# Performance work log

Hardware: AMD Instinct MI355X
Metric: run time of the kernel (lower is better)

The kernel has to match this reference:

```python
import jax, jax.numpy as jnp
import numpy as np

N_VIEWS = 3
N = 20000            # samples per omic view
NT = N_VIEWS * N     # homogeneous node count
E = 800000           # number of edges
R = 6                # num_relations
B = 4                # num_bases
H = 1                # heads
D = 128              # proj_dim == hidden_channels
IN_FEAT = 2000
NUM_LABELS = 5
NEG_SLOPE = 0.2      # PyG leaky_relu default slope


def setup_inputs() -> dict:
    key = jax.random.key(0)
    ks = jax.random.split(key, 16)
    inp = {}
    for i in range(N_VIEWS):
        inp[f"x{i}"] = jax.random.normal(ks[i], (N, IN_FEAT), jnp.float32)
        inp[f"w_proj{i}"] = jax.random.normal(ks[3 + i], (IN_FEAT, D), jnp.float32) / np.sqrt(IN_FEAT)
        inp[f"b_proj{i}"] = jnp.zeros((D,), jnp.float32)
    inp["edge_src"] = jax.random.randint(ks[6], (E,), 0, NT, jnp.int32)
    inp["edge_dst"] = jax.random.randint(ks[7], (E,), 0, NT, jnp.int32)
    inp["edge_type"] = jax.random.randint(ks[8], (E,), 0, R, jnp.int32)
    inp["basis"] = jax.random.normal(ks[9], (B, D, H * D), jnp.float32) / np.sqrt(D)
    inp["comp"] = jax.random.normal(ks[10], (R, B), jnp.float32) / np.sqrt(B)
    inp["att_q"] = jax.random.normal(ks[11], (H * D, H), jnp.float32) / np.sqrt(D)
    inp["att_k"] = jax.random.normal(ks[12], (H * D, H), jnp.float32) / np.sqrt(D)
    inp["conv_bias"] = jnp.zeros((H * D,), jnp.float32)
    inp["w_int"] = jax.random.normal(ks[13], (N_VIEWS * H * D, NUM_LABELS), jnp.float32) / np.sqrt(N_VIEWS * D)
    inp["b_int"] = jnp.zeros((NUM_LABELS,), jnp.float32)
    return inp


def rgat_conv(x, edge_src, edge_dst, edge_type, basis, comp, att_q, att_k, bias):
    """PyG RGATConv: basis-decomposed relational transform + additive
    across-relation self-attention (dim=1), sum aggregation, concat heads."""
    e = edge_src.shape[0]
    # relation weights from bases: [R, D, H*D]
    w = jnp.einsum('rb,bio->rio', comp, basis)
    # transform every node under every relation: [R, NT, H*D]
    xw = jnp.einsum('nd,rdo->rno', x, w)
    xi = xw[edge_type, edge_dst]   # [E, H*D] transformed target feats
    xj = xw[edge_type, edge_src]   # [E, H*D] transformed source feats
    q = xi @ att_q                 # [E, H]
    k = xj @ att_k                 # [E, H]
    alpha = jax.nn.leaky_relu(q + k, NEG_SLOPE)
    # softmax over incoming edges of each target node (across relations)
    amax = jax.lax.stop_gradient(jax.ops.segment_max(alpha, edge_dst, num_segments=NT))
    ealpha = jnp.exp(alpha - amax[edge_dst])
    denom = jax.ops.segment_sum(ealpha, edge_dst, num_segments=NT)
    alpha = ealpha / (denom[edge_dst] + 1e-16)
    msg = (xj.reshape(e, H, D) * alpha[:, :, None]).reshape(e, H * D)
    out = jax.ops.segment_sum(msg, edge_dst, num_segments=NT)  # [NT, H*D]
    return out + bias


def reference(x0, x1, x2, w_proj0, b_proj0, w_proj1, b_proj1, w_proj2, b_proj2,
              edge_src, edge_dst, edge_type, basis, comp, att_q, att_k,
              conv_bias, w_int, b_int):
    # per-omic projection + relu, then concat to homogeneous node matrix
    h = jnp.concatenate([
        jax.nn.relu(x0 @ w_proj0 + b_proj0),
        jax.nn.relu(x1 @ w_proj1 + b_proj1),
        jax.nn.relu(x2 @ w_proj2 + b_proj2),
    ], axis=0)                                        # [NT, D]
    h = jax.nn.relu(rgat_conv(h, edge_src, edge_dst, edge_type,
                              basis, comp, att_q, att_k, conv_bias))
    # node-type gather: nodes are ordered by type in the homogeneous graph
    views = h.reshape(N_VIEWS, N, H * D)              # [V, N, D]
    feat = jnp.transpose(views, (1, 0, 2)).reshape(N, N_VIEWS * H * D)
    # LinearIntegration: concat views -> linear to classes
    return feat @ w_int + b_int                        # [N, NUM_LABELS]
```

## Files before the change

kernel.cpp:

```cpp
#include <hip/hip_runtime.h>
#include <hip/hip_bf16.h>

#define NV 3
#define NN 20000
#define NTT 60000
#define NE 800000
#define NR 6
#define NB 4
#define DD 128
#define INF 2000
#define NL 5

typedef __attribute__((ext_vector_type(8))) short short8;
typedef __attribute__((ext_vector_type(4))) float f32x4;

__device__ __forceinline__ unsigned short f2bf(float f) {
    unsigned int u = __float_as_uint(f);
    u += 0x7FFFu + ((u >> 16) & 1u);
    return (unsigned short)(u >> 16);
}
__device__ __forceinline__ float bf2f(unsigned short h) {
    return __uint_as_float(((unsigned int)h) << 16);
}
__device__ __forceinline__ short8 cvt8(float4 a, float4 b) {
    union { short8 v; __hip_bfloat162 h[4]; } u;
    u.h[0] = __float22bfloat162_rn(make_float2(a.x, a.y));
    u.h[1] = __float22bfloat162_rn(make_float2(a.z, a.w));
    u.h[2] = __float22bfloat162_rn(make_float2(b.x, b.y));
    u.h[3] = __float22bfloat162_rn(make_float2(b.z, b.w));
    return u.v;
}

__global__ void prep_misc(const float* __restrict__ basis, const float* __restrict__ comp,
                          const float* __restrict__ att_q, const float* __restrict__ att_k,
                          unsigned short* __restrict__ wTrel, float* __restrict__ qvec,
                          float* __restrict__ kvec, int* __restrict__ indeg,
                          int* __restrict__ cursor) {
    int b = blockIdx.x;
    if (b < 384) {
        int idx = b * 256 + threadIdx.x;
        int r = idx / (DD * DD);
        int rem = idx - r * (DD * DD);
        int o = rem / DD;
        int d = rem - o * DD;
        float s = 0.f;
        #pragma unroll
        for (int bb = 0; bb < NB; bb++)
            s += comp[r * NB + bb] * basis[((size_t)bb * DD + d) * DD + o];
        wTrel[idx] = f2bf(s);
    } else if (b < 390) {
        int idx = (b - 384) * 256 + threadIdx.x;
        int sel = idx / (NR * DD);
        int rem = idx - sel * (NR * DD);
        int r = rem / DD;
        int d = rem - r * DD;
        const float* att = sel ? att_k : att_q;
        float s = 0.f;
        #pragma unroll
        for (int bb = 0; bb < NB; bb++) {
            float cb = comp[r * NB + bb];
            float t = 0.f;
            for (int o = 0; o < DD; o++) t += basis[((size_t)bb * DD + d) * DD + o] * att[o];
            s += cb * t;
        }
        (sel ? kvec : qvec)[r * DD + d] = s;
    } else {
        int i = (b - 390) * 256 + threadIdx.x;
        if (i < NTT) { indeg[i] = 0; cursor[i] = 0; }
    }
}

__global__ void prep_wTt(const float* __restrict__ w0, const float* __restrict__ w1,
                         const float* __restrict__ w2, unsigned short* __restrict__ wT) {
    __shared__ float tile[32][33];
    int v = blockIdx.z;
    const float* w = (v == 0) ? w0 : ((v == 1) ? w1 : w2);
    int k0 = blockIdx.x * 32, n0 = blockIdx.y * 32;
    int tx = threadIdx.x & 31, ty = threadIdx.x >> 5;
    #pragma unroll
    for (int i = 0; i < 4; i++) {
        int k = k0 + ty + i * 8;
        if (k < INF) tile[ty + i * 8][tx] = w[(size_t)k * DD + n0 + tx];
    }
    __syncthreads();
    #pragma unroll
    for (int i = 0; i < 4; i++) {
        int k = k0 + tx;
        int n = n0 + ty + i * 8;
        if (k < INF)
            wT[(size_t)v * DD * INF + (size_t)n * INF + k] = f2bf(tile[tx][ty + i * 8]);
    }
}

__global__ __launch_bounds__(256) void proj_nl(
    const float* __restrict__ x0, const float* __restrict__ x1, const float* __restrict__ x2,
    const float* __restrict__ b0, const float* __restrict__ b1, const float* __restrict__ b2,
    const unsigned short* __restrict__ wT, unsigned short* __restrict__ hout) {
    int v = blockIdx.y;
    const float* x = (v == 0) ? x0 : ((v == 1) ? x1 : x2);
    const float* bias = (v == 0) ? b0 : ((v == 1) ? b1 : b2);
    const unsigned short* wTv = wT + (size_t)v * DD * INF;

    int t = threadIdx.x, lane = t & 63, wid = t >> 6;
    int wm = wid >> 1, wn = wid & 1;
    int lm = lane & 15, lq = lane >> 4;

    const float* aptr[4];
    #pragma unroll
    for (int i = 0; i < 4; i++) {
        int r = blockIdx.x * 128 + wm * 64 + i * 16 + lm;
        if (r >= NN) r = NN - 1;
        aptr[i] = x + (size_t)r * INF + lq * 8;
    }
    const unsigned short* bptr[4];
    #pragma unroll
    for (int j = 0; j < 4; j++) {
        int c = wn * 64 + j * 16 + lm;
        bptr[j] = wTv + (size_t)c * INF + lq * 8;
    }

    f32x4 acc[4][4];
    #pragma unroll
    for (int i = 0; i < 4; i++)
        #pragma unroll
        for (int j = 0; j < 4; j++) {
            acc[i][j][0] = 0.f; acc[i][j][1] = 0.f; acc[i][j][2] = 0.f; acc[i][j][3] = 0.f;
        }

    #pragma unroll 2
    for (int kk = 0; kk < 62; kk++) {
        short8 af[4], bfr[4];
        #pragma unroll
        for (int i = 0; i < 4; i++) {
            const float4* p = (const float4*)(aptr[i] + kk * 32);
            af[i] = cvt8(p[0], p[1]);
        }
        #pragma unroll
        for (int j = 0; j < 4; j++)
            bfr[j] = *(const short8*)(bptr[j] + kk * 32);
        #pragma unroll
        for (int i = 0; i < 4; i++)
            #pragma unroll
            for (int j = 0; j < 4; j++)
                acc[i][j] = __builtin_amdgcn_mfma_f32_16x16x32_bf16(af[i], bfr[j], acc[i][j], 0, 0, 0);
    }
    {
        short8 af[4], bfr[4];
        short8 z = {0, 0, 0, 0, 0, 0, 0, 0};
        #pragma unroll
        for (int i = 0; i < 4; i++) {
            if (lq < 2) {
                const float4* p = (const float4*)(aptr[i] + 62 * 32);
                af[i] = cvt8(p[0], p[1]);
            } else af[i] = z;
        }
        #pragma unroll
        for (int j = 0; j < 4; j++)
            bfr[j] = (lq < 2) ? *(const short8*)(bptr[j] + 62 * 32) : z;
        #pragma unroll
        for (int i = 0; i < 4; i++)
            #pragma unroll
            for (int j = 0; j < 4; j++)
                acc[i][j] = __builtin_amdgcn_mfma_f32_16x16x32_bf16(af[i], bfr[j], acc[i][j], 0, 0, 0);
    }
    #pragma unroll
    for (int i = 0; i < 4; i++) {
        int lr = wm * 64 + i * 16 + lq * 4;
        #pragma unroll
        for (int j = 0; j < 4; j++) {
            int c = wn * 64 + j * 16 + lm;
            float bv = bias[c];
            #pragma unroll
            for (int u = 0; u < 4; u++) {
                int grow = blockIdx.x * 128 + lr + u;
                if (grow < NN) {
                    float o = fmaxf(acc[i][j][u] + bv, 0.f);
                    hout[((size_t)(v * NN + grow)) * DD + c] = f2bf(o);
                }
            }
        }
    }
}

__global__ __launch_bounds__(256) void xw_nl(
    const unsigned short* __restrict__ h, const unsigned short* __restrict__ wTrel,
    unsigned short* __restrict__ xw) {
    int r = blockIdx.y;
    const unsigned short* wTr = wTrel + (size_t)r * DD * DD;
    int t = threadIdx.x, lane = t & 63, wid = t >> 6;
    int wm = wid >> 1, wn = wid & 1;
    int lm = lane & 15, lq = lane >> 4;

    const unsigned short* aptr[4];
    #pragma unroll
    for (int i = 0; i < 4; i++) {
        int rr = blockIdx.x * 128 + wm * 64 + i * 16 + lm;
        if (rr >= NTT) rr = NTT - 1;
        aptr[i] = h + (size_t)rr * DD + lq * 8;
    }
    const unsigned short* bptr[4];
    #pragma unroll
    for (int j = 0; j < 4; j++) {
        int c = wn * 64 + j * 16 + lm;
        bptr[j] = wTr + (size_t)c * DD + lq * 8;
    }

    f32x4 acc[4][4];
    #pragma unroll
    for (int i = 0; i < 4; i++)
        #pragma unroll
        for (int j = 0; j < 4; j++) {
            acc[i][j][0] = 0.f; acc[i][j][1] = 0.f; acc[i][j][2] = 0.f; acc[i][j][3] = 0.f;
        }

    #pragma unroll
    for (int kk = 0; kk < 4; kk++) {
        short8 af[4], bfr[4];
        #pragma unroll
        for (int i = 0; i < 4; i++) af[i] = *(const short8*)(aptr[i] + kk * 32);
        #pragma unroll
        for (int j = 0; j < 4; j++) bfr[j] = *(const short8*)(bptr[j] + kk * 32);
        #pragma unroll
        for (int i = 0; i < 4; i++)
            #pragma unroll
            for (int j = 0; j < 4; j++)
                acc[i][j] = __builtin_amdgcn_mfma_f32_16x16x32_bf16(af[i], bfr[j], acc[i][j], 0, 0, 0);
    }
    #pragma unroll
    for (int i = 0; i < 4; i++) {
        int lr = wm * 64 + i * 16 + lq * 4;
        #pragma unroll
        for (int j = 0; j < 4; j++) {
            int c = wn * 64 + j * 16 + lm;
            #pragma unroll
            for (int u = 0; u < 4; u++) {
                int g2 = blockIdx.x * 128 + lr + u;
                if (g2 < NTT)
                    xw[((size_t)r * NTT + g2) * DD + c] = f2bf(acc[i][j][u]);
            }
        }
    }
}

__global__ void qk_nodes(const unsigned short* __restrict__ h, const float* __restrict__ qvec,
                         const float* __restrict__ kvec, float* __restrict__ qn,
                         float* __restrict__ kn) {
    int wid = threadIdx.x >> 6, lane = threadIdx.x & 63;
    int node = blockIdx.x * 4 + wid;
    if (node >= NTT) return;
    unsigned int u = *(const unsigned int*)(h + (size_t)node * DD + lane * 2);
    float h0 = bf2f(u & 0xffff), h1 = bf2f(u >> 16);
    #pragma unroll
    for (int r = 0; r < NR; r++) {
        float pq = h0 * qvec[r * DD + lane * 2] + h1 * qvec[r * DD + lane * 2 + 1];
        float pk = h0 * kvec[r * DD + lane * 2] + h1 * kvec[r * DD + lane * 2 + 1];
        #pragma unroll
        for (int off = 32; off; off >>= 1) {
            pq += __shfl_xor(pq, off);
            pk += __shfl_xor(pk, off);
        }
        if (lane == 0) {
            qn[r * NTT + node] = pq;
            kn[r * NTT + node] = pk;
        }
    }
}

__global__ void hist(const int* __restrict__ dst, int* __restrict__ indeg) {
    int e = blockIdx.x * 256 + threadIdx.x;
    if (e < NE) atomicAdd(&indeg[dst[e]], 1);
}

__global__ __launch_bounds__(1024) void scan_indeg(const int* __restrict__ indeg,
                                                   int* __restrict__ start) {
    int t = threadIdx.x;
    const int per = (NTT + 1023) / 1024;
    int base = t * per;
    int s = 0;
    for (int i = 0; i < per; i++) {
        int idx = base + i;
        if (idx < NTT) s += indeg[idx];
    }
    int lane = t & 63, wid = t >> 6;
    __shared__ int wsum[16];
    int v = s;
    #pragma unroll
    for (int off = 1; off < 64; off <<= 1) {
        int u = __shfl_up(v, off);
        if (lane >= off) v += u;
    }
    if (lane == 63) wsum[wid] = v;
    __syncthreads();
    if (t < 16) {
        int w = wsum[t];
        #pragma unroll
        for (int off = 1; off < 16; off <<= 1) {
            int u = __shfl_up(w, off);
            if (t >= off) w += u;
        }
        wsum[t] = w;
    }
    __syncthreads();
    int excl = (v - s) + (wid ? wsum[wid - 1] : 0);
    int run = excl;
    for (int i = 0; i < per; i++) {
        int idx = base + i;
        if (idx < NTT) {
            start[idx] = run;
            run += indeg[idx];
        }
    }
    if (t == 1023) start[NTT] = run;
}

__global__ void scatter2(const int* __restrict__ dst, const int* __restrict__ src,
                         const int* __restrict__ typ, const int* __restrict__ start,
                         int* __restrict__ cursor, const float* __restrict__ qn,
                         const float* __restrict__ kn, unsigned int* __restrict__ packed,
                         float* __restrict__ wl) {
    int e = blockIdx.x * 256 + threadIdx.x;
    if (e >= NE) return;
    int d = dst[e], ss = src[e], tt = typ[e];
    float al = qn[tt * NTT + d] + kn[tt * NTT + ss];
    al = (al > 0.f) ? al : 0.2f * al;
    float w = __expf(al);
    int pos = atomicAdd(&cursor[d], 1);
    int idx = start[d] + pos;
    packed[idx] = (unsigned)ss | ((unsigned)tt << 16);
    wl[idx] = w;
}

__global__ void aggregate(const unsigned int* __restrict__ packed, const float* __restrict__ wl,
                          const int* __restrict__ start, const unsigned short* __restrict__ xw,
                          const float* __restrict__ conv_bias, float* __restrict__ h2) {
    int wid = threadIdx.x >> 6, lane = threadIdx.x & 63;
    int node = blockIdx.x * 4 + wid;
    if (node >= NTT) return;
    int s0 = start[node], s1 = start[node + 1];
    float a0 = 0.f, a1 = 0.f, denom = 0.f;
    for (int base = s0; base < s1; base += 64) {
        int cnt = min(64, s1 - base);
        unsigned pk = 0;
        float wv = 0.f;
        if (lane < cnt) {
            pk = packed[base + lane];
            wv = wl[base + lane];
        }
        denom += wv;
        for (int i = 0; i < cnt; i++) {
            unsigned sp = __shfl(pk, i);
            float sw = __shfl(wv, i);
            unsigned ss = sp & 0xFFFFu;
            unsigned tt = sp >> 16;
            unsigned u = *(const unsigned int*)(xw + ((size_t)tt * NTT + ss) * DD + lane * 2);
            a0 += sw * bf2f(u & 0xffff);
            a1 += sw * bf2f(u >> 16);
        }
    }
    #pragma unroll
    for (int off = 32; off; off >>= 1) denom += __shfl_xor(denom, off);
    float rdenom = 1.f / (denom + 1e-16f);
    float2 o;
    o.x = fmaxf(a0 * rdenom + conv_bias[lane * 2], 0.f);
    o.y = fmaxf(a1 * rdenom + conv_bias[lane * 2 + 1], 0.f);
    *(float2*)&h2[(size_t)node * DD + lane * 2] = o;
}

__global__ void final_linear(const float* __restrict__ h2, const float* __restrict__ w_int,
                             const float* __restrict__ b_int, float* __restrict__ out) {
    int wid = threadIdx.x >> 6, lane = threadIdx.x & 63;
    int node = blockIdx.x * 4 + wid;
    if (node >= NN) return;
    float acc[NL] = {0.f, 0.f, 0.f, 0.f, 0.f};
    for (int j = lane; j < NV * DD; j += 64) {
        int v = j >> 7, d = j & 127;
        float f = h2[((size_t)(v * NN + node)) * DD + d];
        #pragma unroll
        for (int c = 0; c < NL; c++) acc[c] += f * w_int[j * NL + c];
    }
    #pragma unroll
    for (int c = 0; c < NL; c++) {
        float s = acc[c];
        #pragma unroll
        for (int off = 32; off; off >>= 1) s += __shfl_xor(s, off);
        if (lane == 0) out[(size_t)node * NL + c] = s + b_int[c];
    }
}

extern "C" void kernel_launch(void* const* d_in, const int* in_sizes, int n_in, void* d_out,
                              int out_size, void* d_ws, size_t ws_size, hipStream_t stream) {
    (void)in_sizes; (void)n_in; (void)out_size; (void)ws_size;
    const float* x0 = (const float*)d_in[0];
    const float* w0 = (const float*)d_in[1];
    const float* b0 = (const float*)d_in[2];
    const float* x1 = (const float*)d_in[3];
    const float* w1 = (const float*)d_in[4];
    const float* b1 = (const float*)d_in[5];
    const float* x2 = (const float*)d_in[6];
    const float* w2 = (const float*)d_in[7];
    const float* b2 = (const float*)d_in[8];
    const int* esrc = (const int*)d_in[9];
    const int* edst = (const int*)d_in[10];
    const int* etype = (const int*)d_in[11];
    const float* basis = (const float*)d_in[12];
    const float* comp = (const float*)d_in[13];
    const float* att_q = (const float*)d_in[14];
    const float* att_k = (const float*)d_in[15];
    const float* conv_bias = (const float*)d_in[16];
    const float* w_int = (const float*)d_in[17];
    const float* b_int = (const float*)d_in[18];

    char* ws = (char*)d_ws;
    size_t off = 0;
    auto alloc = [&](size_t bytes) -> void* {
        void* p = ws + off;
        off += bytes;
        off = (off + 255) & ~(size_t)255;
        return p;
    };
    unsigned short* h = (unsigned short*)alloc((size_t)NTT * DD * 2);
    unsigned short* xw = (unsigned short*)alloc((size_t)NR * NTT * DD * 2);
    float* qn = (float*)alloc((size_t)NR * NTT * 4);
    float* kn = (float*)alloc((size_t)NR * NTT * 4);
    unsigned short* wT = (unsigned short*)alloc((size_t)NV * DD * INF * 2);
    unsigned short* wTrel = (unsigned short*)alloc((size_t)NR * DD * DD * 2);
    float* qvec = (float*)alloc((size_t)NR * DD * 4);
    float* kvec = (float*)alloc((size_t)NR * DD * 4);
    int* indeg = (int*)alloc((size_t)NTT * 4);
    int* cursor = (int*)alloc((size_t)NTT * 4);
    int* startp = (int*)alloc((size_t)(NTT + 1) * 4);
    unsigned int* packed = (unsigned int*)alloc((size_t)NE * 4);
    float* wl = (float*)alloc((size_t)NE * 4);
    float* h2 = (float*)alloc((size_t)NTT * DD * 4);

    prep_misc<<<390 + (NTT + 255) / 256, 256, 0, stream>>>(basis, comp, att_q, att_k, wTrel,
                                                           qvec, kvec, indeg, cursor);
    prep_wTt<<<dim3((INF + 31) / 32, DD / 32, NV), 256, 0, stream>>>(w0, w1, w2, wT);
    hist<<<(NE + 255) / 256, 256, 0, stream>>>(edst, indeg);
    scan_indeg<<<1, 1024, 0, stream>>>(indeg, startp);

    proj_nl<<<dim3((NN + 127) / 128, NV), 256, 0, stream>>>(x0, x1, x2, b0, b1, b2, wT, h);
    qk_nodes<<<(NTT + 3) / 4, 256, 0, stream>>>(h, qvec, kvec, qn, kn);
    xw_nl<<<dim3((NTT + 127) / 128, NR), 256, 0, stream>>>(h, wTrel, xw);

    scatter2<<<(NE + 255) / 256, 256, 0, stream>>>(edst, esrc, etype, startp, cursor, qn, kn,
                                                   packed, wl);
    aggregate<<<(NTT + 3) / 4, 256, 0, stream>>>(packed, wl, startp, xw, conv_bias, h2);
    final_linear<<<(NN + 3) / 4, 256, 0, stream>>>(h2, w_int, b_int, (float*)d_out);
}
```

Before: 948.2 us.

## Halve projection tile rows, prefetch A registers, and coalesce indegree scan

The projection GEMM now uses 64-row blocks instead of 128, doubling the grid (about 939 blocks vs 471) so more CUs stay busy. The fp32 A-operand loads are software-prefetched one k-step ahead in registers to hide global latency behind the MFMAs. The single-block indegree scan is rewritten to process 1024 contiguous elements per round, so loads and stores are coalesced instead of strided per thread. In exchange, each B fragment is reused across fewer rows, which raises weight reads, and the scan adds extra barriers per round.

```diff
diff --git a/kernel.cpp b/kernel.cpp
--- a/kernel.cpp
+++ b/kernel.cpp
@@ -105,10 +105,10 @@
     int wm = wid >> 1, wn = wid & 1;
     int lm = lane & 15, lq = lane >> 4;
 
-    const float* aptr[4];
-    #pragma unroll
-    for (int i = 0; i < 4; i++) {
-        int r = blockIdx.x * 128 + wm * 64 + i * 16 + lm;
+    const float* aptr[2];
+    #pragma unroll
+    for (int i = 0; i < 2; i++) {
+        int r = blockIdx.x * 64 + wm * 32 + i * 16 + lm;
         if (r >= NN) r = NN - 1;
         aptr[i] = x + (size_t)r * INF + lq * 8;
     }
@@ -119,36 +119,46 @@
         bptr[j] = wTv + (size_t)c * INF + lq * 8;
     }
 
-    f32x4 acc[4][4];
-    #pragma unroll
-    for (int i = 0; i < 4; i++)
+    f32x4 acc[2][4];
+    #pragma unroll
+    for (int i = 0; i < 2; i++)
         #pragma unroll
         for (int j = 0; j < 4; j++) {
             acc[i][j][0] = 0.f; acc[i][j][1] = 0.f; acc[i][j][2] = 0.f; acc[i][j][3] = 0.f;
         }
 
-    #pragma unroll 2
+    float4 pa[2][2];
+    #pragma unroll
+    for (int i = 0; i < 2; i++) {
+        const float4* p = (const float4*)aptr[i];
+        pa[i][0] = p[0]; pa[i][1] = p[1];
+    }
+
     for (int kk = 0; kk < 62; kk++) {
-        short8 af[4], bfr[4];
-        #pragma unroll
-        for (int i = 0; i < 4; i++) {
-            const float4* p = (const float4*)(aptr[i] + kk * 32);
-            af[i] = cvt8(p[0], p[1]);
-        }
+        short8 bfr[4];
         #pragma unroll
         for (int j = 0; j < 4; j++)
             bfr[j] = *(const short8*)(bptr[j] + kk * 32);
-        #pragma unroll
-        for (int i = 0; i < 4; i++)
+        short8 af[2];
+        #pragma unroll
+        for (int i = 0; i < 2; i++) af[i] = cvt8(pa[i][0], pa[i][1]);
+        int nk = (kk + 1 < 62) ? kk + 1 : 0;
+        #pragma unroll
+        for (int i = 0; i < 2; i++) {
+            const float4* p = (const float4*)(aptr[i] + nk * 32);
+            pa[i][0] = p[0]; pa[i][1] = p[1];
+        }
+        #pragma unroll
+        for (int i = 0; i < 2; i++)
             #pragma unroll
             for (int j = 0; j < 4; j++)
                 acc[i][j] = __builtin_amdgcn_mfma_f32_16x16x32_bf16(af[i], bfr[j], acc[i][j], 0, 0, 0);
     }
     {
-        short8 af[4], bfr[4];
+        short8 af[2], bfr[4];
         short8 z = {0, 0, 0, 0, 0, 0, 0, 0};
         #pragma unroll
-        for (int i = 0; i < 4; i++) {
+        for (int i = 0; i < 2; i++) {
             if (lq < 2) {
                 const float4* p = (const float4*)(aptr[i] + 62 * 32);
                 af[i] = cvt8(p[0], p[1]);
@@ -158,21 +168,21 @@
         for (int j = 0; j < 4; j++)
             bfr[j] = (lq < 2) ? *(const short8*)(bptr[j] + 62 * 32) : z;
         #pragma unroll
-        for (int i = 0; i < 4; i++)
+        for (int i = 0; i < 2; i++)
             #pragma unroll
             for (int j = 0; j < 4; j++)
                 acc[i][j] = __builtin_amdgcn_mfma_f32_16x16x32_bf16(af[i], bfr[j], acc[i][j], 0, 0, 0);
     }
     #pragma unroll
-    for (int i = 0; i < 4; i++) {
-        int lr = wm * 64 + i * 16 + lq * 4;
+    for (int i = 0; i < 2; i++) {
+        int lr = wm * 32 + i * 16 + lq * 4;
         #pragma unroll
         for (int j = 0; j < 4; j++) {
             int c = wn * 64 + j * 16 + lm;
             float bv = bias[c];
             #pragma unroll
             for (int u = 0; u < 4; u++) {
-                int grow = blockIdx.x * 128 + lr + u;
+                int grow = blockIdx.x * 64 + lr + u;
                 if (grow < NN) {
                     float o = fmaxf(acc[i][j][u] + bv, 0.f);
                     hout[((size_t)(v * NN + grow)) * DD + c] = f2bf(o);
@@ -273,44 +283,37 @@
 
 __global__ __launch_bounds__(1024) void scan_indeg(const int* __restrict__ indeg,
                                                    int* __restrict__ start) {
-    int t = threadIdx.x;
-    const int per = (NTT + 1023) / 1024;
-    int base = t * per;
-    int s = 0;
-    for (int i = 0; i < per; i++) {
-        int idx = base + i;
-        if (idx < NTT) s += indeg[idx];
-    }
-    int lane = t & 63, wid = t >> 6;
     __shared__ int wsum[16];
-    int v = s;
-    #pragma unroll
-    for (int off = 1; off < 64; off <<= 1) {
-        int u = __shfl_up(v, off);
-        if (lane >= off) v += u;
-    }
-    if (lane == 63) wsum[wid] = v;
-    __syncthreads();
-    if (t < 16) {
-        int w = wsum[t];
-        #pragma unroll
-        for (int off = 1; off < 16; off <<= 1) {
-            int u = __shfl_up(w, off);
-            if (t >= off) w += u;
-        }
-        wsum[t] = w;
-    }
-    __syncthreads();
-    int excl = (v - s) + (wid ? wsum[wid - 1] : 0);
-    int run = excl;
-    for (int i = 0; i < per; i++) {
-        int idx = base + i;
-        if (idx < NTT) {
-            start[idx] = run;
-            run += indeg[idx];
-        }
-    }
-    if (t == 1023) start[NTT] = run;
+    int t = threadIdx.x, lane = t & 63, wid = t >> 6;
+    int running = 0;
+    const int ROUNDS = (NTT + 1023) / 1024;
+    for (int round = 0; round < ROUNDS; round++) {
+        int idx = round * 1024 + t;
+        int v = (idx < NTT) ? indeg[idx] : 0;
+        int incl = v;
+        #pragma unroll
+        for (int off = 1; off < 64; off <<= 1) {
+            int u = __shfl_up(incl, off);
+            if (lane >= off) incl += u;
+        }
+        if (lane == 63) wsum[wid] = incl;
+        __syncthreads();
+        if (t < 16) {
+            int w = wsum[t];
+            #pragma unroll
+            for (int off = 1; off < 16; off <<= 1) {
+                int u = __shfl_up(w, off);
+                if (t >= off) w += u;
+            }
+            wsum[t] = w;
+        }
+        __syncthreads();
+        int excl = running + (incl - v) + (wid ? wsum[wid - 1] : 0);
+        if (idx < NTT) start[idx] = excl;
+        running += wsum[15];
+        __syncthreads();
+    }
+    if (t == 0) start[NTT] = running;
 }
 
 __global__ void scatter2(const int* __restrict__ dst, const int* __restrict__ src,
@@ -439,7 +442,7 @@
     hist<<<(NE + 255) / 256, 256, 0, stream>>>(edst, indeg);
     scan_indeg<<<1, 1024, 0, stream>>>(indeg, startp);
 
-    proj_nl<<<dim3((NN + 127) / 128, NV), 256, 0, stream>>>(x0, x1, x2, b0, b1, b2, wT, h);
+    proj_nl<<<dim3((NN + 63) / 64, NV), 256, 0, stream>>>(x0, x1, x2, b0, b1, b2, wT, h);
     qk_nodes<<<(NTT + 3) / 4, 256, 0, stream>>>(h, qvec, kvec, qn, kn);
     xw_nl<<<dim3((NTT + 127) / 128, NR), 256, 0, stream>>>(h, wTrel, xw);
 
```

New measurement: 958.2 us. Within noise of the previous version (+1.1%).
